# Optimization experiments

Hardware: AMD Instinct MI355X
Metric: run time of the kernel (lower is better)

The kernel has to match this reference:

```python
import jax, jax.numpy as jnp
import numpy as np
import math

N, E, NF, BF, H, NH, DEPTH = 2048, 65536, 128, 16, 512, 8, 5
HD = H // NH

def _lin(key, fan_in, fan_out):
    k1, k2 = jax.random.split(key)
    W = jax.random.normal(k1, (fan_in, fan_out), jnp.float32) * math.sqrt(2.0 / fan_out)
    b = jnp.zeros((fan_out,), jnp.float32)
    return W, b

def setup_inputs() -> dict:
    key = jax.random.key(0)
    ks = jax.random.split(key, 12)
    x = jax.random.normal(ks[0], (N, NF), jnp.float32)
    edge_index = jax.random.randint(ks[1], (2, E), 0, N, jnp.int64)
    edge_attr = jax.random.normal(ks[2], (E, BF), jnp.float32)
    Wn, bn = _lin(ks[3], NF, H)
    We, be = _lin(ks[4], BF, NH)
    Wq, bq = _lin(ks[5], H, H)
    Wk, bk = _lin(ks[6], H, H)
    Wv, bv = _lin(ks[7], H, H)
    Wo, bo = _lin(ks[8], H, H)
    W1, b1 = _lin(ks[9], H, 4 * H)
    W2, b2 = _lin(ks[10], 4 * H, H)
    g1 = jnp.ones((H,), jnp.float32); be1 = jnp.zeros((H,), jnp.float32)
    g2 = jnp.ones((H,), jnp.float32); be2 = jnp.zeros((H,), jnp.float32)
    return dict(x=x, edge_index=edge_index, edge_attr=edge_attr,
                Wn=Wn, bn=bn, We=We, be=be, Wq=Wq, bq=bq, Wk=Wk, bk=bk,
                Wv=Wv, bv=bv, Wo=Wo, bo=bo, W1=W1, b1=b1, W2=W2, b2=b2,
                g1=g1, be1=be1, g2=g2, be2=be2)

def _ln(x, g, b, eps=1e-5):
    m = jnp.mean(x, axis=-1, keepdims=True)
    v = jnp.var(x, axis=-1, keepdims=True)
    return (x - m) * jax.lax.rsqrt(v + eps) * g + b

def reference(x, edge_index, edge_attr, Wn, bn, We, be, Wq, bq, Wk, bk,
              Wv, bv, Wo, bo, W1, b1, W2, b2, g1, be1, g2, be2):
    h = x @ Wn + bn                                   # [N, H]
    e_bias = edge_attr @ We + be                      # [E, NH]
    src, dst = edge_index[0], edge_index[1]
    bias = jnp.zeros((NH, N, N), jnp.float32).at[:, src, dst].set(e_bias.T)
    scale = 1.0 / math.sqrt(HD)
    for _ in range(DEPTH):
        Q = (h @ Wq + bq).reshape(N, NH, HD).transpose(1, 0, 2)   # [h, n, d]
        K = (h @ Wk + bk).reshape(N, NH, HD).transpose(1, 0, 2)
        V = (h @ Wv + bv).reshape(N, NH, HD).transpose(1, 0, 2)
        scores = jnp.einsum('hnd,hmd->hnm', Q, K) * scale + bias  # [h, n, m]
        attn = jax.nn.softmax(scores, axis=-1)
        out = jnp.einsum('hnm,hmd->hnd', attn, V)                 # [h, n, d]
        out = out.transpose(1, 0, 2).reshape(N, H) @ Wo + bo
        h = _ln(h + out, g1, be1)
        h_ff = jnp.maximum(h @ W1 + b1, 0.0) @ W2 + b2
        h = _ln(h + h_ff, g2, be2)
    return h
```

## Files before the change

kernel.cpp:

```cpp
#include <hip/hip_runtime.h>
#include <hip/hip_bf16.h>

#define NN 2048
#define EE 65536
#define NF_ 128
#define HH 512
#define NHH 8
#define HD 64
#define DEPTH 5
#define KSPLIT 3
#define NTILE_TOT (NN / 64)
#define LOG2E 1.4426950408889634f

typedef __attribute__((ext_vector_type(8))) short bf16x8;
typedef __attribute__((ext_vector_type(4))) float f32x4;

__device__ __forceinline__ ushort f2bf(float x) {
    uint u = __builtin_bit_cast(uint, x);
    u += 0x7fffu + ((u >> 16) & 1u);
    return (ushort)(u >> 16);
}

#define GLD16(gp, lp)                                                          \
    __builtin_amdgcn_global_load_lds(                                          \
        (const __attribute__((address_space(1))) unsigned int*)(gp),           \
        (__attribute__((address_space(3))) unsigned int*)(lp), 16, 0, 0)

template<int BM, int BN, int OUT, int RELU>
__global__ __launch_bounds__(256) void gemm_mfma(const ushort* __restrict__ A,
                                                 const ushort* __restrict__ Bt,
                                                 const float* __restrict__ bias,
                                                 float* __restrict__ C,
                                                 ushort* __restrict__ Cb,
                                                 ushort* __restrict__ qb,
                                                 ushort* __restrict__ kb,
                                                 ushort* __restrict__ vtb,
                                                 int M, int N, int K) {
    constexpr int WM = BM / 2, WN = BN / 2;
    constexpr int MR = BM / 32, NR = BN / 32;
    __shared__ __align__(16) ushort As[2][BM * 64];
    __shared__ __align__(16) ushort Bs[2][BN * 64];
    const int t = threadIdx.x;
    const int w = t >> 6, l = t & 63;
    const int wr = w >> 1, wc = w & 1;
    const int m0 = blockIdx.y * BM, n0 = blockIdx.x * BN;

    f32x4 acc[MR][NR];
#pragma unroll
    for (int m = 0; m < MR; ++m)
#pragma unroll
        for (int n = 0; n < NR; ++n) acc[m][n] = (f32x4){0.f, 0.f, 0.f, 0.f};

    const int srow = t >> 3, sch = t & 7;
    auto stage = [&](int buf, int kt) {
#pragma unroll
        for (int r = 0; r < MR; ++r) {
            int rr = r * 32 + srow;
            int c = sch ^ (rr & 7);
            GLD16(A + (size_t)(m0 + rr) * K + kt * 64 + c * 8,
                  &As[buf][rr * 64 + sch * 8]);
        }
#pragma unroll
        for (int r = 0; r < NR; ++r) {
            int rr = r * 32 + srow;
            int c = sch ^ (rr & 7);
            GLD16(Bt + (size_t)(n0 + rr) * K + kt * 64 + c * 8,
                  &Bs[buf][rr * 64 + sch * 8]);
        }
    };

    stage(0, 0);
    const int NT = K / 64;
    for (int kt = 0; kt < NT; ++kt) {
        __syncthreads();
        if (kt + 1 < NT) stage((kt + 1) & 1, kt + 1);
        const int buf = kt & 1;
#pragma unroll
        for (int kk = 0; kk < 2; ++kk) {
            bf16x8 af[MR], bfr[NR];
#pragma unroll
            for (int m = 0; m < MR; ++m) {
                int R = wr * WM + m * 16 + (l & 15);
                int c = kk * 4 + (l >> 4);
                af[m] = *(const bf16x8*)&As[buf][R * 64 + (c ^ (R & 7)) * 8];
            }
#pragma unroll
            for (int n = 0; n < NR; ++n) {
                int R = wc * WN + n * 16 + (l & 15);
                int c = kk * 4 + (l >> 4);
                bfr[n] = *(const bf16x8*)&Bs[buf][R * 64 + (c ^ (R & 7)) * 8];
            }
#pragma unroll
            for (int m = 0; m < MR; ++m)
#pragma unroll
                for (int n = 0; n < NR; ++n)
                    acc[m][n] = __builtin_amdgcn_mfma_f32_16x16x32_bf16(af[m], bfr[n], acc[m][n], 0, 0, 0);
        }
    }

#pragma unroll
    for (int m = 0; m < MR; ++m) {
        int row = m0 + wr * WM + m * 16 + (l >> 4) * 4;
#pragma unroll
        for (int n = 0; n < NR; ++n) {
            int col = n0 + wc * WN + n * 16 + (l & 15);
            float bv = bias[col];
#pragma unroll
            for (int j = 0; j < 4; ++j) {
                float vv = acc[m][n][j] + bv;
                if (RELU) vv = fmaxf(vv, 0.f);
                int r = row + j;
                if (OUT == 0) {
                    C[(size_t)r * N + col] = vv;
                } else if (OUT == 1) {
                    C[(size_t)r * N + col] = vv;
                    Cb[(size_t)r * N + col] = f2bf(vv);
                } else if (OUT == 2) {
                    Cb[(size_t)r * N + col] = f2bf(vv);
                } else {
                    int type = col >> 9, head = (col >> 6) & 7, dd = col & 63;
                    ushort bv16 = f2bf(vv);
                    if (type == 0) qb[((size_t)head * NN + r) * 64 + dd] = bv16;
                    else if (type == 1) kb[((size_t)head * NN + r) * 64 + dd] = bv16;
                    else vtb[((size_t)head * 64 + dd) * NN + r] = bv16;
                }
            }
        }
    }
}

__global__ __launch_bounds__(256) void xcvt(const float* __restrict__ x, ushort* __restrict__ xb, int n) {
    int i = blockIdx.x * 256 + threadIdx.x;
    if (i < n) xb[i] = f2bf(x[i]);
}

__global__ __launch_bounds__(256) void wtrans(const float* __restrict__ W, ushort* __restrict__ WT,
                                              int K, int N, int rowoff) {
    __shared__ float tile[32][33];
    int n0 = blockIdx.x * 32, k0 = blockIdx.y * 32;
    int tc = threadIdx.x & 31, tr = threadIdx.x >> 5;
#pragma unroll
    for (int i = 0; i < 32; i += 8) tile[tr + i][tc] = W[(size_t)(k0 + tr + i) * N + n0 + tc];
    __syncthreads();
#pragma unroll
    for (int i = 0; i < 32; i += 8)
        WT[(size_t)(rowoff + n0 + tr + i) * K + k0 + tc] = f2bf(tile[tc][tr + i]);
}

__global__ __launch_bounds__(256) void bconcat(const float* __restrict__ a, const float* __restrict__ b,
                                               const float* __restrict__ c, float* __restrict__ o) {
    int i = blockIdx.x * 256 + threadIdx.x;
    if (i < 1536) o[i] = i < 512 ? a[i] : (i < 1024 ? b[i - 512] : c[i - 1024]);
}

__global__ __launch_bounds__(256) void ebias_kernel(const float* __restrict__ ea,
                                                    const float* __restrict__ We,
                                                    const float* __restrict__ be,
                                                    float* __restrict__ eb) {
    int e = blockIdx.x * 256 + threadIdx.x;
    float a[16];
#pragma unroll
    for (int i = 0; i < 16; ++i) a[i] = ea[(size_t)e * 16 + i];
#pragma unroll
    for (int j = 0; j < 8; ++j) {
        float s = be[j];
#pragma unroll
        for (int i = 0; i < 16; ++i) s += a[i] * We[i * 8 + j];
        eb[(size_t)e * 8 + j] = s;
    }
}

__global__ __launch_bounds__(256) void amax_kernel(const int* __restrict__ eidx, int* __restrict__ lastE) {
    int e = blockIdx.x * 256 + threadIdx.x;
    int s = eidx[e], d = eidx[EE + e];
    atomicMax(&lastE[s * NN + d], e);
}

__global__ __launch_bounds__(256) void count_kernel(const int* __restrict__ eidx,
                                                    const int* __restrict__ lastE,
                                                    int* __restrict__ cnt) {
    int e = blockIdx.x * 256 + threadIdx.x;
    int s = eidx[e], d = eidx[EE + e];
    if (lastE[s * NN + d] == e) atomicAdd(&cnt[s], 1);
}

__global__ __launch_bounds__(256) void scan2048(const int* __restrict__ cnt,
                                                int* __restrict__ rowptr) {
    __shared__ int sums[256];
    int t = threadIdx.x;
    int loc[8];
    int s = 0;
#pragma unroll
    for (int i = 0; i < 8; ++i) { loc[i] = s; s += cnt[t * 8 + i]; }
    sums[t] = s;
    __syncthreads();
    for (int off = 1; off < 256; off <<= 1) {
        int v = (t >= off) ? sums[t - off] : 0;
        __syncthreads();
        sums[t] += v;
        __syncthreads();
    }
    int base = (t == 0) ? 0 : sums[t - 1];
#pragma unroll
    for (int i = 0; i < 8; ++i) rowptr[t * 8 + i] = base + loc[i];
    if (t == 255) rowptr[NN] = sums[255];
}

__global__ __launch_bounds__(256) void rt_count(const int* __restrict__ eidx,
                                                const int* __restrict__ lastE,
                                                int* __restrict__ cnt2) {
    int e = blockIdx.x * 256 + threadIdx.x;
    int s = eidx[e], d = eidx[EE + e];
    if (lastE[s * NN + d] == e) atomicAdd(&cnt2[s * NTILE_TOT + (d >> 6)], 1);
}

__global__ __launch_bounds__(256) void rt_scan(const int* __restrict__ rowptr,
                                               const int* __restrict__ cnt2,
                                               int* __restrict__ rtptr,
                                               int* __restrict__ rtoff) {
    int row = blockIdx.x * 256 + threadIdx.x;
    if (row >= NN) return;
    int base = rowptr[row];
#pragma unroll
    for (int t = 0; t < NTILE_TOT; ++t) {
        rtptr[row * NTILE_TOT + t] = base;
        rtoff[row * NTILE_TOT + t] = base;
        base += cnt2[row * NTILE_TOT + t];
    }
    if (row == NN - 1) rtptr[NN * NTILE_TOT] = base;
}

__global__ __launch_bounds__(256) void rt_fill(const int* __restrict__ eidx,
                                               const int* __restrict__ lastE,
                                               const float* __restrict__ eb,
                                               int* __restrict__ rtoff,
                                               int* __restrict__ csr_dst,
                                               float* __restrict__ csr_b) {
    int e = blockIdx.x * 256 + threadIdx.x;
    int s = eidx[e], d = eidx[EE + e];
    if (lastE[s * NN + d] == e) {
        int pos = atomicAdd(&rtoff[s * NTILE_TOT + (d >> 6)], 1);
        csr_dst[pos] = d & 63;
#pragma unroll
        for (int j = 0; j < 8; ++j) csr_b[(size_t)pos * 8 + j] = eb[(size_t)e * 8 + j] * LOG2E;
    }
}

__global__ __launch_bounds__(256) void attn_mfma(const ushort* __restrict__ qb,
                                                 const ushort* __restrict__ kb,
                                                 const ushort* __restrict__ vtb,
                                                 const int* __restrict__ rtptr,
                                                 const int* __restrict__ csr_dst,
                                                 const float* __restrict__ csr_b,
                                                 float* __restrict__ opart,
                                                 float* __restrict__ Mp,
                                                 float* __restrict__ Sp) {
    const int id = blockIdx.x;
    const int f = (id & 7) * 96 + (id >> 3);
    const int n0 = (f & 31) * 64;
    const int head = (f >> 5) & 7;
    const int ks = f >> 8;
    const int tstart = (ks * 32) / 3, tend = ((ks + 1) * 32) / 3;
    const int t = threadIdx.x;
    const int w = t >> 6, l = t & 63;
    const int lq = l & 15, lg = l >> 4;
    const float c1 = 0.125f * LOG2E;

    __shared__ __align__(16) ushort Ks2[2][64 * 64];
    __shared__ __align__(16) ushort Vs2[2][64 * 64];
    __shared__ int Rt[64][12];

    bf16x8 qf0, qf1;
    {
        int r = n0 + w * 16 + lq;
        const ushort* qp = qb + ((size_t)head * NN + r) * HD + lg * 8;
        qf0 = *(const bf16x8*)qp;
        qf1 = *(const bf16x8*)(qp + 32);
    }
    const int ntile = tend - tstart;
    for (int i = t; i < 64 * 12; i += 256) {
        int r = i / 12, c = i % 12;
        if (c <= ntile) Rt[r][c] = rtptr[(n0 + r) * NTILE_TOT + tstart + c];
    }
    float M = -1e30f, S = 0.f;
    f32x4 o[4];
#pragma unroll
    for (int db = 0; db < 4; ++db) o[db] = (f32x4){0.f, 0.f, 0.f, 0.f};

    auto stageK = [&](int buf, int tile) {
        int m0k = tile * 64;
#pragma unroll
        for (int s = 0; s < 2; ++s) {
            int slot = t + s * 256;
            int rr = slot >> 3, blk = slot & 7, sb = blk ^ (rr & 7);
            GLD16(kb + ((size_t)head * NN + m0k + rr) * 64 + sb * 8,
                  &Ks2[buf][rr * 64 + blk * 8]);
        }
    };
    auto stageV = [&](int buf, int tile) {
        int m0k = tile * 64;
#pragma unroll
        for (int s = 0; s < 2; ++s) {
            int slot = t + s * 256;
            int rr = slot >> 3, blk = slot & 7, sb = blk ^ (rr & 7);
            GLD16(vtb + ((size_t)head * 64 + rr) * NN + m0k + sb * 8,
                  &Vs2[buf][rr * 64 + blk * 8]);
        }
    };

    stageK(0, tstart);
    stageV(0, tstart);
    __syncthreads();

    const int sl0 = (((lg << 1) + 0) & 3) * 16 + lq;
    const int sl1 = (((lg << 1) + 1) & 3) * 16 + lq;
    const int hi = lg & 2;

    for (int tt = tstart; tt < tend; ++tt) {
        const int tl = tt - tstart;
        const int cb = tl & 1;
        if (tt + 1 < tend) { stageK(cb ^ 1, tt + 1); stageV(cb ^ 1, tt + 1); }

        f32x4 vv[4];
        {
            const ushort* Kb_ = &Ks2[cb][0];
            __builtin_amdgcn_s_setprio(1);
#pragma unroll
            for (int b = 0; b < 4; ++b) {
                int key = b * 16 + lq;
                bf16x8 k0 = *(const bf16x8*)&Kb_[key * 64 + ((lg ^ (key & 7)) * 8)];
                bf16x8 k1 = *(const bf16x8*)&Kb_[key * 64 + (((lg + 4) ^ (key & 7)) * 8)];
                f32x4 s_ = {0.f, 0.f, 0.f, 0.f};
                s_ = __builtin_amdgcn_mfma_f32_16x16x32_bf16(k0, qf0, s_, 0, 0, 0);
                s_ = __builtin_amdgcn_mfma_f32_16x16x32_bf16(k1, qf1, s_, 0, 0, 0);
                vv[b] = s_;
            }
            __builtin_amdgcn_s_setprio(0);
        }
#pragma unroll
        for (int b = 0; b < 4; ++b)
#pragma unroll
            for (int j = 0; j < 4; ++j) vv[b][j] *= c1;

        {
            int rq = w * 16 + lq;
            int p0 = Rt[rq][tl], p1 = Rt[rq][tl + 1];
            for (int e = p0; e < p1; ++e) {
                int dd = csr_dst[e];
                if (((dd >> 2) & 3) == lg) {
                    float bv = csr_b[(size_t)e * 8 + head];
#pragma unroll
                    for (int b = 0; b < 4; ++b)
#pragma unroll
                        for (int j = 0; j < 4; ++j)
                            vv[b][j] += (b == (dd >> 4) && j == (dd & 3)) ? bv : 0.f;
                }
            }
        }

        float mx = vv[0][0];
#pragma unroll
        for (int b = 0; b < 4; ++b)
#pragma unroll
            for (int j = 0; j < 4; ++j) mx = fmaxf(mx, vv[b][j]);
        mx = fmaxf(mx, __shfl_xor(mx, 16, 64));
        mx = fmaxf(mx, __shfl_xor(mx, 32, 64));
        float Mn = fmaxf(M, mx);
        float fr = exp2f(M - Mn);
        float ts = 0.f;
#pragma unroll
        for (int b = 0; b < 4; ++b)
#pragma unroll
            for (int j = 0; j < 4; ++j) { vv[b][j] = exp2f(vv[b][j] - Mn); ts += vv[b][j]; }
        ts += __shfl_xor(ts, 16, 64);
        ts += __shfl_xor(ts, 32, 64);
        S = S * fr + ts;
        M = Mn;

        uint U0, U1, U2, U3, U4, U5, U6, U7;
        asm("v_cvt_pk_bf16_f32 %0, %1, %2" : "=v"(U0) : "v"(vv[0][0]), "v"(vv[0][1]));
        asm("v_cvt_pk_bf16_f32 %0, %1, %2" : "=v"(U1) : "v"(vv[0][2]), "v"(vv[0][3]));
        asm("v_cvt_pk_bf16_f32 %0, %1, %2" : "=v"(U2) : "v"(vv[1][0]), "v"(vv[1][1]));
        asm("v_cvt_pk_bf16_f32 %0, %1, %2" : "=v"(U3) : "v"(vv[1][2]), "v"(vv[1][3]));
        asm("v_cvt_pk_bf16_f32 %0, %1, %2" : "=v"(U4) : "v"(vv[2][0]), "v"(vv[2][1]));
        asm("v_cvt_pk_bf16_f32 %0, %1, %2" : "=v"(U5) : "v"(vv[2][2]), "v"(vv[2][3]));
        asm("v_cvt_pk_bf16_f32 %0, %1, %2" : "=v"(U6) : "v"(vv[3][0]), "v"(vv[3][1]));
        asm("v_cvt_pk_bf16_f32 %0, %1, %2" : "=v"(U7) : "v"(vv[3][2]), "v"(vv[3][3]));

        uint ra, rb;
        ra = (uint)__shfl((int)U0, sl0); rb = (uint)__shfl((int)U2, sl0);
        uint p00 = hi ? rb : ra;
        ra = (uint)__shfl((int)U1, sl0); rb = (uint)__shfl((int)U3, sl0);
        uint p01 = hi ? rb : ra;
        ra = (uint)__shfl((int)U0, sl1); rb = (uint)__shfl((int)U2, sl1);
        uint p02 = hi ? rb : ra;
        ra = (uint)__shfl((int)U1, sl1); rb = (uint)__shfl((int)U3, sl1);
        uint p03 = hi ? rb : ra;
        ra = (uint)__shfl((int)U4, sl0); rb = (uint)__shfl((int)U6, sl0);
        uint p10 = hi ? rb : ra;
        ra = (uint)__shfl((int)U5, sl0); rb = (uint)__shfl((int)U7, sl0);
        uint p11 = hi ? rb : ra;
        ra = (uint)__shfl((int)U4, sl1); rb = (uint)__shfl((int)U6, sl1);
        uint p12 = hi ? rb : ra;
        ra = (uint)__shfl((int)U5, sl1); rb = (uint)__shfl((int)U7, sl1);
        uint p13 = hi ? rb : ra;
        uint4 pu0 = {p00, p01, p02, p03};
        uint4 pu1 = {p10, p11, p12, p13};
        bf16x8 pa0 = __builtin_bit_cast(bf16x8, pu0);
        bf16x8 pa1 = __builtin_bit_cast(bf16x8, pu1);

#pragma unroll
        for (int j = 0; j < 4; ++j) {
            float Fj = __shfl(fr, lg * 4 + j, 64);
            o[0][j] *= Fj; o[1][j] *= Fj; o[2][j] *= Fj; o[3][j] *= Fj;
        }

        {
            const ushort* Vb_ = &Vs2[cb][0];
            __builtin_amdgcn_s_setprio(1);
#pragma unroll
            for (int db = 0; db < 4; ++db) {
                int dim = db * 16 + lq;
                bf16x8 v0 = *(const bf16x8*)&Vb_[dim * 64 + ((lg ^ (dim & 7)) * 8)];
                bf16x8 v1 = *(const bf16x8*)&Vb_[dim * 64 + (((lg + 4) ^ (dim & 7)) * 8)];
                o[db] = __builtin_amdgcn_mfma_f32_16x16x32_bf16(pa0, v0, o[db], 0, 0, 0);
                o[db] = __builtin_amdgcn_mfma_f32_16x16x32_bf16(pa1, v1, o[db], 0, 0, 0);
            }
            __builtin_amdgcn_s_setprio(0);
        }
        __syncthreads();
    }

#pragma unroll
    for (int db = 0; db < 4; ++db)
#pragma unroll
        for (int j = 0; j < 4; ++j) {
            int r = n0 + w * 16 + lg * 4 + j;
            opart[((size_t)ks * NN + r) * HH + head * HD + db * 16 + lq] = o[db][j];
        }
    if (l < 16) {
        int r = n0 + w * 16 + l;
        Mp[((size_t)ks * NHH + head) * NN + r] = M;
        Sp[((size_t)ks * NHH + head) * NN + r] = S;
    }
}

__global__ __launch_bounds__(256) void attn_combine(const float* __restrict__ opart,
                                                    const float* __restrict__ Mp,
                                                    const float* __restrict__ Sp,
                                                    ushort* __restrict__ aob) {
    int i = blockIdx.x * 256 + threadIdx.x;
    int row = i >> 9, col = i & 511;
    int head = col >> 6;
    float m0 = Mp[(size_t)head * NN + row];
    float m1 = Mp[((size_t)NHH + head) * NN + row];
    float m2 = Mp[((size_t)2 * NHH + head) * NN + row];
    float s0 = Sp[(size_t)head * NN + row];
    float s1 = Sp[((size_t)NHH + head) * NN + row];
    float s2 = Sp[((size_t)2 * NHH + head) * NN + row];
    float m = fmaxf(m0, fmaxf(m1, m2));
    float w0 = exp2f(m0 - m), w1 = exp2f(m1 - m), w2 = exp2f(m2 - m);
    float num = opart[(size_t)row * HH + col] * w0
              + opart[((size_t)NN + row) * HH + col] * w1
              + opart[((size_t)2 * NN + row) * HH + col] * w2;
    float den = s0 * w0 + s1 * w1 + s2 * w2;
    aob[i] = f2bf(num / den);
}

template<int BF16OUT>
__global__ __launch_bounds__(256) void ln_kernel(const float* __restrict__ a,
                                                 const float* __restrict__ b,
                                                 const float* __restrict__ g,
                                                 const float* __restrict__ be,
                                                 float* __restrict__ out,
                                                 ushort* __restrict__ outb) {
    int row = blockIdx.x * 4 + (threadIdx.x >> 6);
    int lane = threadIdx.x & 63;
    const float* pa = a + (size_t)row * HH;
    const float* pb = b + (size_t)row * HH;
    float x[8];
    float s = 0.f;
#pragma unroll
    for (int i = 0; i < 8; ++i) { x[i] = pa[lane + i * 64] + pb[lane + i * 64]; s += x[i]; }
#pragma unroll
    for (int off = 32; off > 0; off >>= 1) s += __shfl_xor(s, off, 64);
    float mean = s * (1.f / 512.f);
    float vs = 0.f;
#pragma unroll
    for (int i = 0; i < 8; ++i) { float d = x[i] - mean; vs += d * d; }
#pragma unroll
    for (int off = 32; off > 0; off >>= 1) vs += __shfl_xor(vs, off, 64);
    float rs = rsqrtf(vs * (1.f / 512.f) + 1e-5f);
    float* po = out + (size_t)row * HH;
    ushort* pob = outb + (size_t)row * HH;
#pragma unroll
    for (int i = 0; i < 8; ++i) {
        float v = (x[i] - mean) * rs * g[lane + i * 64] + be[lane + i * 64];
        po[lane + i * 64] = v;
        if (BF16OUT) pob[lane + i * 64] = f2bf(v);
    }
}

extern "C" void kernel_launch(void* const* d_in, const int* in_sizes, int n_in,
                              void* d_out, int out_size, void* d_ws, size_t ws_size,
                              hipStream_t stream) {
    const float* x   = (const float*)d_in[0];
    const int*  eidx = (const int*)d_in[1];
    const float* ea  = (const float*)d_in[2];
    const float* Wn = (const float*)d_in[3];  const float* bn = (const float*)d_in[4];
    const float* We = (const float*)d_in[5];  const float* be = (const float*)d_in[6];
    const float* Wq = (const float*)d_in[7];  const float* bq = (const float*)d_in[8];
    const float* Wk = (const float*)d_in[9];  const float* bk = (const float*)d_in[10];
    const float* Wv = (const float*)d_in[11]; const float* bv = (const float*)d_in[12];
    const float* Wo = (const float*)d_in[13]; const float* bo = (const float*)d_in[14];
    const float* W1 = (const float*)d_in[15]; const float* b1 = (const float*)d_in[16];
    const float* W2 = (const float*)d_in[17]; const float* b2 = (const float*)d_in[18];
    const float* g1 = (const float*)d_in[19]; const float* be1 = (const float*)d_in[20];
    const float* g2 = (const float*)d_in[21]; const float* be2 = (const float*)d_in[22];
    float* out = (float*)d_out;

    char* base = (char*)d_ws;
    size_t off = 0;
    auto carve = [&](size_t bytes) { void* p = base + off; off = (off + bytes + 255) & ~(size_t)255; return p; };
    float*  h    = (float*)carve((size_t)NN * HH * 4);
    ushort* hb   = (ushort*)carve((size_t)NN * HH * 2);
    float*  po   = (float*)carve((size_t)NN * HH * 4);
    ushort* ff1b = (ushort*)carve((size_t)NN * 4 * HH * 2);
    ushort* qb   = (ushort*)carve((size_t)NN * HH * 2);
    ushort* kbf  = (ushort*)carve((size_t)NN * HH * 2);
    ushort* vtb  = (ushort*)carve((size_t)NN * HH * 2);
    ushort* aob  = (ushort*)carve((size_t)NN * HH * 2);
    ushort* xb   = (ushort*)carve((size_t)NN * NF_ * 2);
    ushort* WnT  = (ushort*)carve((size_t)HH * NF_ * 2);
    ushort* WqkvT= (ushort*)carve((size_t)3 * HH * HH * 2);
    ushort* WoT  = (ushort*)carve((size_t)HH * HH * 2);
    ushort* W1T  = (ushort*)carve((size_t)4 * HH * HH * 2);
    ushort* W2T  = (ushort*)carve((size_t)4 * HH * HH * 2);
    float*  bqkv = (float*)carve((size_t)3 * HH * 4);
    float*  eb   = (float*)carve((size_t)EE * NHH * 4);
    float*  csr_b= (float*)carve((size_t)EE * NHH * 4);
    float*  Mp   = (float*)carve((size_t)KSPLIT * NHH * NN * 4);
    float*  Sp   = (float*)carve((size_t)KSPLIT * NHH * NN * 4);
    int* cnt     = (int*)carve((size_t)NN * 4);
    int* rowptr  = (int*)carve((size_t)(NN + 1) * 4);
    int* csr_dst = (int*)carve((size_t)EE * 4);
    int* cnt2    = (int*)carve((size_t)NN * NTILE_TOT * 4);
    int* rtptr   = (int*)carve((size_t)(NN * NTILE_TOT + 1) * 4);
    int* rtoff   = (int*)carve((size_t)NN * NTILE_TOT * 4);
    int* lastE = (int*)po;
    float* opart = (float*)po;

    hipMemsetAsync(lastE, 0xFF, (size_t)NN * NN * 4, stream);
    hipMemsetAsync(cnt, 0, (size_t)NN * 4, stream);
    hipMemsetAsync(cnt2, 0, (size_t)NN * NTILE_TOT * 4, stream);

    xcvt<<<(NN * NF_ + 255) / 256, 256, 0, stream>>>(x, xb, NN * NF_);
    wtrans<<<dim3(HH / 32, NF_ / 32), 256, 0, stream>>>(Wn, WnT, NF_, HH, 0);
    wtrans<<<dim3(HH / 32, HH / 32), 256, 0, stream>>>(Wq, WqkvT, HH, HH, 0);
    wtrans<<<dim3(HH / 32, HH / 32), 256, 0, stream>>>(Wk, WqkvT, HH, HH, 512);
    wtrans<<<dim3(HH / 32, HH / 32), 256, 0, stream>>>(Wv, WqkvT, HH, HH, 1024);
    wtrans<<<dim3(HH / 32, HH / 32), 256, 0, stream>>>(Wo, WoT, HH, HH, 0);
    wtrans<<<dim3(4 * HH / 32, HH / 32), 256, 0, stream>>>(W1, W1T, HH, 4 * HH, 0);
    wtrans<<<dim3(HH / 32, 4 * HH / 32), 256, 0, stream>>>(W2, W2T, 4 * HH, HH, 0);
    bconcat<<<6, 256, 0, stream>>>(bq, bk, bv, bqkv);

    ebias_kernel<<<EE / 256, 256, 0, stream>>>(ea, We, be, eb);
    amax_kernel<<<EE / 256, 256, 0, stream>>>(eidx, lastE);
    count_kernel<<<EE / 256, 256, 0, stream>>>(eidx, lastE, cnt);
    scan2048<<<1, 256, 0, stream>>>(cnt, rowptr);
    rt_count<<<EE / 256, 256, 0, stream>>>(eidx, lastE, cnt2);
    rt_scan<<<NN / 256, 256, 0, stream>>>(rowptr, cnt2, rtptr, rtoff);
    rt_fill<<<EE / 256, 256, 0, stream>>>(eidx, lastE, eb, rtoff, csr_dst, csr_b);

    gemm_mfma<64, 64, 1, 0><<<dim3(HH / 64, NN / 64), 256, 0, stream>>>(
        xb, WnT, bn, h, hb, nullptr, nullptr, nullptr, NN, HH, NF_);

    for (int d = 0; d < DEPTH; ++d) {
        gemm_mfma<64, 64, 3, 0><<<dim3(3 * HH / 64, NN / 64), 256, 0, stream>>>(
            hb, WqkvT, bqkv, nullptr, nullptr, qb, kbf, vtb, NN, 3 * HH, HH);
        attn_mfma<<<dim3(32 * NHH * KSPLIT), 256, 0, stream>>>(
            qb, kbf, vtb, rtptr, csr_dst, csr_b, opart, Mp, Sp);
        attn_combine<<<NN * HH / 256, 256, 0, stream>>>(opart, Mp, Sp, aob);
        gemm_mfma<32, 64, 0, 0><<<dim3(HH / 64, NN / 32), 256, 0, stream>>>(
            aob, WoT, bo, po, nullptr, nullptr, nullptr, nullptr, NN, HH, HH);
        ln_kernel<1><<<NN / 4, 256, 0, stream>>>(h, po, g1, be1, h, hb);
        gemm_mfma<64, 64, 2, 1><<<dim3(4 * HH / 64, NN / 64), 256, 0, stream>>>(
            hb, W1T, b1, nullptr, ff1b, nullptr, nullptr, nullptr, NN, 4 * HH, HH);
        gemm_mfma<32, 64, 0, 0><<<dim3(HH / 64, NN / 32), 256, 0, stream>>>(
            ff1b, W2T, b2, po, nullptr, nullptr, nullptr, nullptr, NN, HH, 4 * HH);
        float* dst = (d == DEPTH - 1) ? out : h;
        ln_kernel<1><<<NN / 4, 256, 0, stream>>>(h, po, g2, be2, dst, hb);
    }
    (void)in_sizes; (void)n_in; (void)out_size; (void)ws_size;
}
```

Measured before the change: 626.7 us.

## Fold softmax scale into Q, add LDS edge-bias scatter, skip redundant rescales

Q is pre-scaled by 1/sqrt(d)*log2e when the QKV GEMM writes it, which removes the per-tile score multiply inside attention. A new template variant scatters each tile's sparse edge biases into a per-wave bf16 LDS tile and adds them with vector loads, replacing the per-lane CSR loop. The online-softmax rescale of O and S now runs only when some lane's running max increases. The host alternates the LDS-bias and CSR variants across layers, which looks like an A/B experiment. The LDS path rounds the biases to bf16, and the zero/scatter/read of Bb has no barrier or wave fence between its steps.

```diff
diff --git a/kernel.cpp b/kernel.cpp
--- a/kernel.cpp
+++ b/kernel.cpp
@@ -11,6 +11,7 @@
 #define KSPLIT 3
 #define NTILE_TOT (NN / 64)
 #define LOG2E 1.4426950408889634f
+#define QSCALE 0.18033688011112042f
 
 typedef __attribute__((ext_vector_type(8))) short bf16x8;
 typedef __attribute__((ext_vector_type(4))) float f32x4;
@@ -119,10 +120,9 @@
                     Cb[(size_t)r * N + col] = f2bf(vv);
                 } else {
                     int type = col >> 9, head = (col >> 6) & 7, dd = col & 63;
-                    ushort bv16 = f2bf(vv);
-                    if (type == 0) qb[((size_t)head * NN + r) * 64 + dd] = bv16;
-                    else if (type == 1) kb[((size_t)head * NN + r) * 64 + dd] = bv16;
-                    else vtb[((size_t)head * 64 + dd) * NN + r] = bv16;
+                    if (type == 0) qb[((size_t)head * NN + r) * 64 + dd] = f2bf(vv * QSCALE);
+                    else if (type == 1) kb[((size_t)head * NN + r) * 64 + dd] = f2bf(vv);
+                    else vtb[((size_t)head * 64 + dd) * NN + r] = f2bf(vv);
                 }
             }
         }
@@ -246,6 +246,7 @@
     }
 }
 
+template<int BIASLDS>
 __global__ __launch_bounds__(256) void attn_mfma(const ushort* __restrict__ qb,
                                                  const ushort* __restrict__ kb,
                                                  const ushort* __restrict__ vtb,
@@ -264,10 +265,10 @@
     const int t = threadIdx.x;
     const int w = t >> 6, l = t & 63;
     const int lq = l & 15, lg = l >> 4;
-    const float c1 = 0.125f * LOG2E;
 
     __shared__ __align__(16) ushort Ks2[2][64 * 64];
     __shared__ __align__(16) ushort Vs2[2][64 * 64];
+    __shared__ __align__(16) ushort Bb[4][16 * 72];
     __shared__ int Rt[64][12];
 
     bf16x8 qf0, qf1;
@@ -320,6 +321,18 @@
         const int tl = tt - tstart;
         const int cb = tl & 1;
         if (tt + 1 < tend) { stageK(cb ^ 1, tt + 1); stageV(cb ^ 1, tt + 1); }
+
+        const int rq = w * 16 + lq;
+        const int p0 = Rt[rq][tl], p1 = Rt[rq][tl + 1];
+
+        if (BIASLDS) {
+            for (int i = l; i < 144; i += 64)
+                *(uint4*)&Bb[w][i * 8] = (uint4){0, 0, 0, 0};
+            if (lg == 0) {
+                for (int e = p0; e < p1; ++e)
+                    Bb[w][lq * 72 + csr_dst[e]] = f2bf(csr_b[(size_t)e * 8 + head]);
+            }
+        }
 
         f32x4 vv[4];
         {
@@ -337,14 +350,17 @@
             }
             __builtin_amdgcn_s_setprio(0);
         }
-#pragma unroll
-        for (int b = 0; b < 4; ++b)
-#pragma unroll
-            for (int j = 0; j < 4; ++j) vv[b][j] *= c1;
-
-        {
-            int rq = w * 16 + lq;
-            int p0 = Rt[rq][tl], p1 = Rt[rq][tl + 1];
+
+        if (BIASLDS) {
+#pragma unroll
+            for (int b = 0; b < 4; ++b) {
+                uint2 bb = *(const uint2*)&Bb[w][lq * 72 + b * 16 + lg * 4];
+                vv[b][0] += __builtin_bit_cast(float, bb.x << 16);
+                vv[b][1] += __builtin_bit_cast(float, bb.x & 0xffff0000u);
+                vv[b][2] += __builtin_bit_cast(float, bb.y << 16);
+                vv[b][3] += __builtin_bit_cast(float, bb.y & 0xffff0000u);
+            }
+        } else {
             for (int e = p0; e < p1; ++e) {
                 int dd = csr_dst[e];
                 if (((dd >> 2) & 3) == lg) {
@@ -365,17 +381,25 @@
             for (int j = 0; j < 4; ++j) mx = fmaxf(mx, vv[b][j]);
         mx = fmaxf(mx, __shfl_xor(mx, 16, 64));
         mx = fmaxf(mx, __shfl_xor(mx, 32, 64));
-        float Mn = fmaxf(M, mx);
-        float fr = exp2f(M - Mn);
+        if (!__all(mx <= M)) {
+            float Mn = fmaxf(M, mx);
+            float fr = exp2f(M - Mn);
+            M = Mn;
+            S *= fr;
+#pragma unroll
+            for (int j = 0; j < 4; ++j) {
+                float Fj = __shfl(fr, lg * 4 + j, 64);
+                o[0][j] *= Fj; o[1][j] *= Fj; o[2][j] *= Fj; o[3][j] *= Fj;
+            }
+        }
         float ts = 0.f;
 #pragma unroll
         for (int b = 0; b < 4; ++b)
 #pragma unroll
-            for (int j = 0; j < 4; ++j) { vv[b][j] = exp2f(vv[b][j] - Mn); ts += vv[b][j]; }
+            for (int j = 0; j < 4; ++j) { vv[b][j] = exp2f(vv[b][j] - M); ts += vv[b][j]; }
         ts += __shfl_xor(ts, 16, 64);
         ts += __shfl_xor(ts, 32, 64);
-        S = S * fr + ts;
-        M = Mn;
+        S += ts;
 
         uint U0, U1, U2, U3, U4, U5, U6, U7;
         asm("v_cvt_pk_bf16_f32 %0, %1, %2" : "=v"(U0) : "v"(vv[0][0]), "v"(vv[0][1]));
@@ -408,12 +432,6 @@
         uint4 pu1 = {p10, p11, p12, p13};
         bf16x8 pa0 = __builtin_bit_cast(bf16x8, pu0);
         bf16x8 pa1 = __builtin_bit_cast(bf16x8, pu1);
-
-#pragma unroll
-        for (int j = 0; j < 4; ++j) {
-            float Fj = __shfl(fr, lg * 4 + j, 64);
-            o[0][j] *= Fj; o[1][j] *= Fj; o[2][j] *= Fj; o[3][j] *= Fj;
-        }
 
         {
             const ushort* Vb_ = &Vs2[cb][0];
@@ -578,8 +596,12 @@
     for (int d = 0; d < DEPTH; ++d) {
         gemm_mfma<64, 64, 3, 0><<<dim3(3 * HH / 64, NN / 64), 256, 0, stream>>>(
             hb, WqkvT, bqkv, nullptr, nullptr, qb, kbf, vtb, NN, 3 * HH, HH);
-        attn_mfma<<<dim3(32 * NHH * KSPLIT), 256, 0, stream>>>(
-            qb, kbf, vtb, rtptr, csr_dst, csr_b, opart, Mp, Sp);
+        if (d & 1)
+            attn_mfma<0><<<dim3(32 * NHH * KSPLIT), 256, 0, stream>>>(
+                qb, kbf, vtb, rtptr, csr_dst, csr_b, opart, Mp, Sp);
+        else
+            attn_mfma<1><<<dim3(32 * NHH * KSPLIT), 256, 0, stream>>>(
+                qb, kbf, vtb, rtptr, csr_dst, csr_b, opart, Mp, Sp);
         attn_combine<<<NN * HH / 256, 256, 0, stream>>>(opart, Mp, Sp, aob);
         gemm_mfma<32, 64, 0, 0><<<dim3(HH / 64, NN / 32), 256, 0, stream>>>(
             aob, WoT, bo, po, nullptr, nullptr, nullptr, nullptr, NN, HH, HH);
```

Result: faster. 596.5 us (-4.8%).
